# Performance work log

Measured on AMD Instinct MI355X. Metric: run time of the kernel, lower is better.

Reference implementation:

```python
import jax, jax.numpy as jnp
import numpy as np

N, L, H, V = 8192, 512, 64, 50000
NUM_PARENT = 1024


def setup_inputs() -> dict:
    key = jax.random.key(0)
    ks = jax.random.split(key, 12)
    def mat(k, shape):
        return 0.1 * jax.random.normal(k, shape, dtype=jnp.float32)
    return {
        "x_word": jax.random.normal(ks[0], (N, L), dtype=jnp.float32),
        "x_index": jax.random.randint(ks[1], (N, L), 0, V),
        "tree": jax.random.randint(ks[2], (N, 2), 0, N),
        "num_parent": NUM_PARENT,
        "embedding": mat(ks[3], (V, H)),
        "W_z": mat(ks[4], (H, H)),
        "U_z": mat(ks[5], (H, H)),
        "b_z": jnp.zeros((H,), dtype=jnp.float32),
        "W_r": mat(ks[6], (H, H)),
        "U_r": mat(ks[7], (H, H)),
        "b_r": jnp.zeros((H,), dtype=jnp.float32),
        "W_h": mat(ks[8], (H, H)),
        "U_h": mat(ks[9], (H, H)),
        "b_h": jnp.zeros((H,), dtype=jnp.float32),
    }


def _hard_sigmoid(x):
    # torch double-threshold trick == clip(0.2*x + 0.5, 0, 1)
    return jnp.clip(0.2 * x + 0.5, 0.0, 1.0)


def reference(x_word, x_index, tree, num_parent, embedding,
              W_z, U_z, b_z, W_r, U_r, b_r, W_h, U_h, b_h):
    n_nodes = x_word.shape[0]
    hdim = embedding.shape[1]

    def step(node_h, xs):
        word, idx, info = xs  # word: [L] f32, idx: [L] int, info: [2] int
        parent_h = node_h[info[0]]                 # [H]
        child_xe = embedding[idx].T @ word         # [H] weighted embedding sum
        z = _hard_sigmoid(W_z @ child_xe + U_z @ parent_h + b_z)
        r = _hard_sigmoid(W_r @ child_xe + U_r @ parent_h + b_r)
        c = jnp.tanh(W_h @ child_xe + U_h @ (parent_h * r) + b_h)
        h = z * parent_h + (1.0 - z) * c           # [H]
        return node_h.at[info[1]].set(h), h

    node_h0 = jnp.zeros((n_nodes, hdim), dtype=x_word.dtype)
    # original loops i in range(len(x_word) - 1)
    _, child_hs = jax.lax.scan(step, node_h0,
                               (x_word[:-1], x_index[:-1], tree[:-1]))
    # output = max over child_hs[num_parent-1:]
    return jnp.max(child_hs[num_parent - 1:], axis=0)
```

## Files before the change

### kernel.cpp

```cpp
#include <hip/hip_runtime.h>
#include <math.h>

#define NODES  8192
#define STEPS  8191
#define LW     512
#define H      64
#define VOCAB  50000
#define SWEEPK 4

typedef __attribute__((ext_vector_type(2))) float f32x2;

__global__ void ws_too_small_kernel(float* __restrict__ out) {
    if (threadIdx.x < H) out[threadIdx.x] = -12345.0f;
}

__global__ __launch_bounds__(256)
void cvt_emb(const float* __restrict__ emb, unsigned int* __restrict__ embq) {
    const int total = VOCAB * H / 4;
    for (int i = blockIdx.x * 256 + threadIdx.x; i < total; i += 256 * 256) {
        float4 v = reinterpret_cast<const float4*>(emb)[i];
        int w = 0;
        w = __builtin_amdgcn_cvt_pk_fp8_f32(v.x, v.y, w, false);
        w = __builtin_amdgcn_cvt_pk_fp8_f32(v.z, v.w, w, true);
        embq[i] = (unsigned int)w;
    }
}

__global__ __launch_bounds__(1024)
void build_schedule(const int* __restrict__ tree, int* __restrict__ writers_g,
                    int* __restrict__ pred_g, int* __restrict__ lstart_g,
                    int* __restrict__ order_g) {
    __shared__ int s_off[NODES + 8];
    __shared__ int wsum[16];
    int tid  = threadIdx.x;
    int lane = tid & 63;
    int wv   = tid >> 6;

    for (int i = tid; i < NODES + 8; i += 1024) s_off[i] = 0;
    __syncthreads();
    for (int j = tid; j < STEPS; j += 1024)
        atomicAdd(&s_off[tree[2 * j + 1]], 1);
    __syncthreads();

    {
        int base = tid * 8;
        int v[8], run = 0;
        #pragma unroll
        for (int e = 0; e < 8; ++e) { v[e] = run; run += s_off[base + e]; }
        int x = run;
        #pragma unroll
        for (int d = 1; d < 64; d <<= 1) {
            int y = __shfl_up(x, d, 64);
            if (lane >= d) x += y;
        }
        if (lane == 63) wsum[wv] = x;
        __syncthreads();
        if (wv == 0) {
            int s = (lane < 16) ? wsum[lane] : 0;
            #pragma unroll
            for (int d = 1; d < 16; d <<= 1) {
                int y = __shfl_up(s, d, 64);
                if (lane >= d) s += y;
            }
            if (lane < 16) wsum[lane] = s;
        }
        __syncthreads();
        int wbase = (wv > 0) ? wsum[wv - 1] : 0;
        int tbase = wbase + x - run;
        #pragma unroll
        for (int e = 0; e < 8; ++e) s_off[base + e] = tbase + v[e];
    }
    __syncthreads();

    for (int j = tid; j < STEPS; j += 1024) {
        int v = tree[2 * j + 1];
        int pos = atomicAdd(&s_off[v], 1);
        writers_g[pos] = j;
    }
    __syncthreads();

    int pr[8];
    #pragma unroll
    for (int e = 0; e < 8; ++e) {
        int i = tid + e * 1024;
        int best = -1;
        if (i < STEPS) {
            int v  = tree[2 * i];
            int t1 = s_off[v];
            int t0 = (v > 0) ? s_off[v - 1] : 0;
            for (int t = t0; t < t1; ++t) {
                int j = writers_g[t];
                if (j < i && j > best) best = j;
            }
            pred_g[i] = best;
        }
        pr[e] = best;
    }
    __syncthreads();

    short* jmp = (short*)s_off;
    short* dep = (short*)s_off + NODES;
    #pragma unroll
    for (int e = 0; e < 8; ++e) {
        int i = tid + e * 1024;
        jmp[i] = (short)pr[e];
        dep[i] = (pr[e] >= 0) ? 1 : 0;
    }
    __syncthreads();

    for (int r = 0; r < 13; ++r) {
        short nd[8], nj[8];
        #pragma unroll
        for (int e = 0; e < 8; ++e) {
            int i = tid + e * 1024;
            int j = jmp[i];
            if (j >= 0) { nd[e] = (short)(dep[i] + dep[j]); nj[e] = jmp[j]; }
            else        { nd[e] = dep[i];                   nj[e] = -1;     }
        }
        __syncthreads();
        #pragma unroll
        for (int e = 0; e < 8; ++e) {
            int i = tid + e * 1024;
            dep[i] = nd[e];
            jmp[i] = nj[e];
        }
        __syncthreads();
    }

    int d8[8];
    #pragma unroll
    for (int e = 0; e < 8; ++e) d8[e] = dep[tid + e * 1024];
    __syncthreads();

    int* lcnt = s_off;
    for (int i = tid; i < NODES; i += 1024) lcnt[i] = 0;
    __syncthreads();
    #pragma unroll
    for (int e = 0; e < 8; ++e) {
        int i = tid + e * 1024;
        if (i < STEPS) atomicAdd(&lcnt[d8[e]], 1);
    }
    __syncthreads();
    {
        int base = tid * 8;
        int v[8], run = 0;
        #pragma unroll
        for (int e = 0; e < 8; ++e) { v[e] = run; run += lcnt[base + e]; }
        int x = run;
        #pragma unroll
        for (int d = 1; d < 64; d <<= 1) {
            int y = __shfl_up(x, d, 64);
            if (lane >= d) x += y;
        }
        if (lane == 63) wsum[wv] = x;
        __syncthreads();
        if (wv == 0) {
            int s = (lane < 16) ? wsum[lane] : 0;
            #pragma unroll
            for (int d = 1; d < 16; d <<= 1) {
                int y = __shfl_up(s, d, 64);
                if (lane >= d) s += y;
            }
            if (lane < 16) wsum[lane] = s;
        }
        __syncthreads();
        int wbase = (wv > 0) ? wsum[wv - 1] : 0;
        int tbase = wbase + x - run;
        #pragma unroll
        for (int e = 0; e < 8; ++e) lstart_g[base + e] = tbase + v[e];
        if (tid == 1023) lstart_g[8192] = tbase + run;
    }
    __threadfence_block();
    __syncthreads();

    for (int i = tid; i < NODES; i += 1024) lcnt[i] = 0;
    __syncthreads();
    #pragma unroll
    for (int e = 0; e < 8; ++e) {
        int i = tid + e * 1024;
        if (i < STEPS) {
            int d = d8[e];
            int pos = atomicAdd(&lcnt[d], 1);
            order_g[lstart_g[d] + pos] = i;
        }
    }
}

__global__ __launch_bounds__(256)
void gather_project(const float* __restrict__ xw, const int* __restrict__ xi,
                    const unsigned int* __restrict__ embq,
                    const float* __restrict__ Wz, const float* __restrict__ Wr,
                    const float* __restrict__ Wh,
                    const float* __restrict__ bz, const float* __restrict__ br,
                    const float* __restrict__ bh,
                    const int* __restrict__ pred,
                    float* __restrict__ A, float* __restrict__ child_h) {
    int i    = blockIdx.x;
    int tid  = threadIdx.x;
    int wave = tid >> 6;
    int lane = tid & 63;
    int g16  = lane >> 2;
    int q4   = lane & 3;

    __shared__ float s_w[LW];
    __shared__ int   s_idx[LW];
    __shared__ float part[4][64];
    __shared__ float xe[64];

    {
        float2 w2 = reinterpret_cast<const float2*>(xw + (size_t)i * LW)[tid];
        int2   i2 = reinterpret_cast<const int2*>(xi + (size_t)i * LW)[tid];
        s_w[2 * tid]     = w2.x;
        s_w[2 * tid + 1] = w2.y;
        s_idx[2 * tid]     = i2.x;
        s_idx[2 * tid + 1] = i2.y;
    }
    __syncthreads();

    const uint4* E = reinterpret_cast<const uint4*>(embq);
    int base_l = wave * 128 + g16;

    float acc[16];
    #pragma unroll
    for (int c = 0; c < 16; ++c) acc[c] = 0.f;

    uint4 q[8];
    float wgt[8];
    #pragma unroll
    for (int u = 0; u < 8; ++u) {
        int l   = base_l + u * 16;
        int idx = s_idx[l];
        wgt[u]  = s_w[l];
        q[u]    = E[(size_t)idx * 4 + q4];
    }
    #pragma unroll
    for (int u = 0; u < 8; ++u) {
        float w = wgt[u];
        unsigned int uw[4] = {q[u].x, q[u].y, q[u].z, q[u].w};
        #pragma unroll
        for (int d = 0; d < 4; ++d) {
            f32x2 lo = __builtin_amdgcn_cvt_pk_f32_fp8((int)uw[d], false);
            f32x2 hi = __builtin_amdgcn_cvt_pk_f32_fp8((int)uw[d], true);
            acc[4 * d + 0] = fmaf(w, lo.x, acc[4 * d + 0]);
            acc[4 * d + 1] = fmaf(w, lo.y, acc[4 * d + 1]);
            acc[4 * d + 2] = fmaf(w, hi.x, acc[4 * d + 2]);
            acc[4 * d + 3] = fmaf(w, hi.y, acc[4 * d + 3]);
        }
    }
    #pragma unroll
    for (int c = 0; c < 16; ++c) {
        acc[c] += __shfl_xor(acc[c], 4,  64);
        acc[c] += __shfl_xor(acc[c], 8,  64);
        acc[c] += __shfl_xor(acc[c], 16, 64);
        acc[c] += __shfl_xor(acc[c], 32, 64);
    }
    if (lane < 4) {
        #pragma unroll
        for (int c = 0; c < 16; ++c) part[wave][lane * 16 + c] = acc[c];
    }
    __syncthreads();
    if (tid < 64) xe[tid] = part[0][tid] + part[1][tid] + part[2][tid] + part[3][tid];
    __syncthreads();

    float s = 0.f;
    if (tid < 192) {
        int o = tid & 63;
        const float* W = (tid < 64) ? Wz : (tid < 128 ? Wr : Wh);
        const float* b = (tid < 64) ? bz : (tid < 128 ? br : bh);
        s = b[o];
        #pragma unroll
        for (int j = 0; j < H; j += 4) {
            float4 w4 = *reinterpret_cast<const float4*>(W + (size_t)o * H + j);
            s = fmaf(w4.x, xe[j],     s);
            s = fmaf(w4.y, xe[j + 1], s);
            s = fmaf(w4.z, xe[j + 2], s);
            s = fmaf(w4.w, xe[j + 3], s);
        }
    }
    bool isroot = (pred[i] < 0);
    if (tid < 64)                part[0][tid]       = s;
    if (tid >= 128 && tid < 192) part[1][tid - 128] = s;
    __syncthreads();
    if (isroot) {
        if (tid < 64) {
            float z = fminf(fmaxf(0.2f * part[0][tid] + 0.5f, 0.f), 1.f);
            float c = tanhf(part[1][tid]);
            child_h[(size_t)i * H + tid] = (1.f - z) * c;
        }
    } else {
        if (tid < 192) A[(size_t)i * 192 + tid] = s;
    }
}

__device__ __forceinline__ float rlane(float v, int j) {
    return __int_as_float(__builtin_amdgcn_readlane(__float_as_int(v), j));
}

__device__ __forceinline__ void gru_core(
        int i, int lane, const float* __restrict__ A,
        const int* __restrict__ pred,
        const float* uz, const float* ur, const float* uh,
        float* __restrict__ child_h) {
    int p = pred[i];
    float ph = (p >= 0) ? child_h[(size_t)p * H + lane] : 0.f;
    const float* Ai = A + (size_t)i * 192;
    float az = Ai[lane];
    float ar = Ai[64 + lane];
    float ah = Ai[128 + lane];

    #pragma unroll
    for (int j = 0; j < H; ++j) {
        float s = rlane(ph, j);
        az = fmaf(uz[j], s, az);
        ar = fmaf(ur[j], s, ar);
    }
    float z = fminf(fmaxf(0.2f * az + 0.5f, 0.f), 1.f);
    float r = fminf(fmaxf(0.2f * ar + 0.5f, 0.f), 1.f);
    float phr = ph * r;
    #pragma unroll
    for (int j = 0; j < H; ++j) {
        float s = rlane(phr, j);
        ah = fmaf(uh[j], s, ah);
    }
    float c = tanhf(ah);
    child_h[(size_t)i * H + lane] = z * ph + (1.f - z) * c;
}

__global__ __launch_bounds__(256)
void sweep_lvl(int k, const int* __restrict__ lstart, const int* __restrict__ order,
               const float* __restrict__ A, const int* __restrict__ pred,
               const float* __restrict__ Uz, const float* __restrict__ Ur,
               const float* __restrict__ Uh, float* __restrict__ child_h) {
    int s0 = lstart[k], s1 = lstart[k + 1];
    int wave = (blockIdx.x * blockDim.x + threadIdx.x) >> 6;
    int lane = threadIdx.x & 63;
    if (s0 + wave >= s1) return;

    float uz[H], ur[H], uh[H];
    #pragma unroll
    for (int j = 0; j < H; j += 4) {
        float4 a4 = *reinterpret_cast<const float4*>(Uz + (size_t)lane * H + j);
        uz[j] = a4.x; uz[j+1] = a4.y; uz[j+2] = a4.z; uz[j+3] = a4.w;
        float4 b4 = *reinterpret_cast<const float4*>(Ur + (size_t)lane * H + j);
        ur[j] = b4.x; ur[j+1] = b4.y; ur[j+2] = b4.z; ur[j+3] = b4.w;
        float4 c4 = *reinterpret_cast<const float4*>(Uh + (size_t)lane * H + j);
        uh[j] = c4.x; uh[j+1] = c4.y; uh[j+2] = c4.z; uh[j+3] = c4.w;
    }
    for (int t = s0 + wave; t < s1; t += 512)
        gru_core(order[t], lane, A, pred, uz, ur, uh, child_h);
}

__global__ __launch_bounds__(512)
void tail_block(const int* __restrict__ lstart, const int* __restrict__ order,
                const float* __restrict__ A, const int* __restrict__ pred,
                const float* __restrict__ Uz, const float* __restrict__ Ur,
                const float* __restrict__ Uh, float* __restrict__ child_h) {
    int wave = threadIdx.x >> 6;
    int lane = threadIdx.x & 63;

    float uz[H], ur[H], uh[H];
    #pragma unroll
    for (int j = 0; j < H; j += 4) {
        float4 a4 = *reinterpret_cast<const float4*>(Uz + (size_t)lane * H + j);
        uz[j] = a4.x; uz[j+1] = a4.y; uz[j+2] = a4.z; uz[j+3] = a4.w;
        float4 b4 = *reinterpret_cast<const float4*>(Ur + (size_t)lane * H + j);
        ur[j] = b4.x; ur[j+1] = b4.y; ur[j+2] = b4.z; ur[j+3] = b4.w;
        float4 c4 = *reinterpret_cast<const float4*>(Uh + (size_t)lane * H + j);
        uh[j] = c4.x; uh[j+1] = c4.y; uh[j+2] = c4.z; uh[j+3] = c4.w;
    }

    for (int k = SWEEPK; k < NODES; ++k) {
        int s0 = lstart[k];
        if (s0 >= STEPS) break;
        int s1 = lstart[k + 1];
        for (int t = s0 + wave; t < s1; t += 8)
            gru_core(order[t], lane, A, pred, uz, ur, uh, child_h);
        __syncthreads();
    }
}

__global__ __launch_bounds__(256)
void reduce_partial(const float* __restrict__ child_h,
                    const int* __restrict__ np_ptr,
                    float* __restrict__ partial) {
    int b   = blockIdx.x;
    int tid = threadIdx.x;
    int h   = tid & 63;
    int grp = tid >> 6;
    int np    = *np_ptr;
    int start = np - 1;
    int total = STEPS - start;
    int per   = (total + gridDim.x - 1) / gridDim.x;
    int r0 = start + b * per;
    int r1 = r0 + per; if (r1 > STEPS) r1 = STEPS;
    float m = -INFINITY;
    for (int row = r0 + grp; row < r1; row += 4)
        m = fmaxf(m, child_h[(size_t)row * H + h]);
    __shared__ float sm[4][64];
    sm[grp][h] = m;
    __syncthreads();
    if (tid < 64)
        partial[b * 64 + tid] = fmaxf(fmaxf(sm[0][tid], sm[1][tid]),
                                      fmaxf(sm[2][tid], sm[3][tid]));
}

__global__ void reduce_final(const float* __restrict__ partial,
                             float* __restrict__ out, int nb) {
    int h = threadIdx.x;
    float m = -INFINITY;
    for (int b = 0; b < nb; ++b) m = fmaxf(m, partial[b * 64 + h]);
    out[h] = m;
}

extern "C" void kernel_launch(void* const* d_in, const int* in_sizes, int n_in,
                              void* d_out, int out_size, void* d_ws, size_t ws_size,
                              hipStream_t stream) {
    const float* xw   = (const float*)d_in[0];
    const int*   xi   = (const int*)  d_in[1];
    const int*   tree = (const int*)  d_in[2];
    const int*   np   = (const int*)  d_in[3];
    const float* emb  = (const float*)d_in[4];
    const float* Wz   = (const float*)d_in[5];
    const float* Uz   = (const float*)d_in[6];
    const float* bz   = (const float*)d_in[7];
    const float* Wr   = (const float*)d_in[8];
    const float* Ur   = (const float*)d_in[9];
    const float* br   = (const float*)d_in[10];
    const float* Wh   = (const float*)d_in[11];
    const float* Uh   = (const float*)d_in[12];
    const float* bh   = (const float*)d_in[13];

    size_t bA   = (size_t)STEPS * 192 * 4;
    size_t bCH  = (size_t)STEPS * H   * 4;
    size_t bEH  = (size_t)VOCAB * H   * 1;
    size_t bInt = (size_t)(8192 * 3 + 8256) * 4;
    size_t bPar = 56 * 64 * 4 + 256;
    size_t need = bA + bCH + bEH + bInt + bPar;
    if (ws_size < need) {
        ws_too_small_kernel<<<1, 64, 0, stream>>>((float*)d_out);
        return;
    }

    char* base = (char*)d_ws;
    float*          A       = (float*)base;                 base += bA;
    float*          child_h = (float*)base;                 base += bCH;
    unsigned int*   embq    = (unsigned int*)base;          base += bEH;
    int*            pred    = (int*)base;
    int*            writers = pred    + 8192;
    int*            order   = writers + 8192;
    int*            lstart  = order   + 8192;
    float*          partial = (float*)(lstart + 8256);

    cvt_emb        <<<256, 256, 0, stream>>>(emb, embq);

    build_schedule <<<1,  1024, 0, stream>>>(tree, writers, pred, lstart, order);

    gather_project <<<STEPS, 256, 0, stream>>>(xw, xi, embq, Wz, Wr, Wh,
                                               bz, br, bh, pred, A, child_h);

    for (int k = 1; k < SWEEPK; ++k)
        sweep_lvl  <<<128, 256, 0, stream>>>(k, lstart, order, A, pred,
                                             Uz, Ur, Uh, child_h);
    tail_block     <<<1, 512, 0, stream>>>(lstart, order, A, pred,
                                           Uz, Ur, Uh, child_h);

    reduce_partial <<<56,  256, 0, stream>>>(child_h, np, partial);
    reduce_final   <<<1,    64, 0, stream>>>(partial, (float*)d_out, 56);
}
```

Measured before the change: 288.1 us.

## Overlap schedule construction with gather by merging into one launch

The single-block dependency-schedule build moves into block 0 of the gather/projection kernel, so the serial schedule work runs alongside the 8191 gather blocks instead of before them. Because gather no longer knows pred, it always writes A, and a new root_steps kernel computes root hidden states afterwards. The sweep level count also rises from 4 to 6. The schedule block now runs with only 256 threads and larger per-thread register arrays, which may make that path longer, and it adds one extra launch plus the A reads for roots.

After: 319.9 us. +11.1%, slower.

```diff
diff --git a/kernel.cpp b/kernel.cpp
--- a/kernel.cpp
+++ b/kernel.cpp
@@ -6,7 +6,7 @@
 #define LW     512
 #define H      64
 #define VOCAB  50000
-#define SWEEPK 4
+#define SWEEPK 6
 
 typedef __attribute__((ext_vector_type(2))) float f32x2;
 
@@ -26,186 +26,168 @@
     }
 }
 
-__global__ __launch_bounds__(1024)
-void build_schedule(const int* __restrict__ tree, int* __restrict__ writers_g,
-                    int* __restrict__ pred_g, int* __restrict__ lstart_g,
-                    int* __restrict__ order_g) {
-    __shared__ int s_off[NODES + 8];
-    __shared__ int wsum[16];
-    int tid  = threadIdx.x;
-    int lane = tid & 63;
-    int wv   = tid >> 6;
-
-    for (int i = tid; i < NODES + 8; i += 1024) s_off[i] = 0;
-    __syncthreads();
-    for (int j = tid; j < STEPS; j += 1024)
-        atomicAdd(&s_off[tree[2 * j + 1]], 1);
-    __syncthreads();
-
-    {
-        int base = tid * 8;
-        int v[8], run = 0;
-        #pragma unroll
-        for (int e = 0; e < 8; ++e) { v[e] = run; run += s_off[base + e]; }
-        int x = run;
-        #pragma unroll
-        for (int d = 1; d < 64; d <<= 1) {
-            int y = __shfl_up(x, d, 64);
-            if (lane >= d) x += y;
-        }
-        if (lane == 63) wsum[wv] = x;
-        __syncthreads();
-        if (wv == 0) {
-            int s = (lane < 16) ? wsum[lane] : 0;
-            #pragma unroll
-            for (int d = 1; d < 16; d <<= 1) {
-                int y = __shfl_up(s, d, 64);
-                if (lane >= d) s += y;
-            }
-            if (lane < 16) wsum[lane] = s;
-        }
-        __syncthreads();
-        int wbase = (wv > 0) ? wsum[wv - 1] : 0;
-        int tbase = wbase + x - run;
-        #pragma unroll
-        for (int e = 0; e < 8; ++e) s_off[base + e] = tbase + v[e];
-    }
-    __syncthreads();
-
-    for (int j = tid; j < STEPS; j += 1024) {
-        int v = tree[2 * j + 1];
-        int pos = atomicAdd(&s_off[v], 1);
-        writers_g[pos] = j;
-    }
-    __syncthreads();
-
-    int pr[8];
-    #pragma unroll
-    for (int e = 0; e < 8; ++e) {
-        int i = tid + e * 1024;
-        int best = -1;
-        if (i < STEPS) {
-            int v  = tree[2 * i];
-            int t1 = s_off[v];
-            int t0 = (v > 0) ? s_off[v - 1] : 0;
-            for (int t = t0; t < t1; ++t) {
-                int j = writers_g[t];
-                if (j < i && j > best) best = j;
-            }
-            pred_g[i] = best;
-        }
-        pr[e] = best;
-    }
-    __syncthreads();
-
-    short* jmp = (short*)s_off;
-    short* dep = (short*)s_off + NODES;
-    #pragma unroll
-    for (int e = 0; e < 8; ++e) {
-        int i = tid + e * 1024;
-        jmp[i] = (short)pr[e];
-        dep[i] = (pr[e] >= 0) ? 1 : 0;
-    }
-    __syncthreads();
-
-    for (int r = 0; r < 13; ++r) {
-        short nd[8], nj[8];
-        #pragma unroll
-        for (int e = 0; e < 8; ++e) {
-            int i = tid + e * 1024;
-            int j = jmp[i];
-            if (j >= 0) { nd[e] = (short)(dep[i] + dep[j]); nj[e] = jmp[j]; }
-            else        { nd[e] = dep[i];                   nj[e] = -1;     }
-        }
-        __syncthreads();
-        #pragma unroll
-        for (int e = 0; e < 8; ++e) {
-            int i = tid + e * 1024;
-            dep[i] = nd[e];
-            jmp[i] = nj[e];
-        }
-        __syncthreads();
-    }
-
-    int d8[8];
-    #pragma unroll
-    for (int e = 0; e < 8; ++e) d8[e] = dep[tid + e * 1024];
-    __syncthreads();
-
-    int* lcnt = s_off;
-    for (int i = tid; i < NODES; i += 1024) lcnt[i] = 0;
-    __syncthreads();
-    #pragma unroll
-    for (int e = 0; e < 8; ++e) {
-        int i = tid + e * 1024;
-        if (i < STEPS) atomicAdd(&lcnt[d8[e]], 1);
-    }
-    __syncthreads();
-    {
-        int base = tid * 8;
-        int v[8], run = 0;
-        #pragma unroll
-        for (int e = 0; e < 8; ++e) { v[e] = run; run += lcnt[base + e]; }
-        int x = run;
-        #pragma unroll
-        for (int d = 1; d < 64; d <<= 1) {
-            int y = __shfl_up(x, d, 64);
-            if (lane >= d) x += y;
-        }
-        if (lane == 63) wsum[wv] = x;
-        __syncthreads();
-        if (wv == 0) {
-            int s = (lane < 16) ? wsum[lane] : 0;
-            #pragma unroll
-            for (int d = 1; d < 16; d <<= 1) {
-                int y = __shfl_up(s, d, 64);
-                if (lane >= d) s += y;
-            }
-            if (lane < 16) wsum[lane] = s;
-        }
-        __syncthreads();
-        int wbase = (wv > 0) ? wsum[wv - 1] : 0;
-        int tbase = wbase + x - run;
-        #pragma unroll
-        for (int e = 0; e < 8; ++e) lstart_g[base + e] = tbase + v[e];
-        if (tid == 1023) lstart_g[8192] = tbase + run;
-    }
-    __threadfence_block();
-    __syncthreads();
-
-    for (int i = tid; i < NODES; i += 1024) lcnt[i] = 0;
-    __syncthreads();
-    #pragma unroll
-    for (int e = 0; e < 8; ++e) {
-        int i = tid + e * 1024;
-        if (i < STEPS) {
-            int d = d8[e];
-            int pos = atomicAdd(&lcnt[d], 1);
-            order_g[lstart_g[d] + pos] = i;
-        }
-    }
-}
-
 __global__ __launch_bounds__(256)
-void gather_project(const float* __restrict__ xw, const int* __restrict__ xi,
-                    const unsigned int* __restrict__ embq,
-                    const float* __restrict__ Wz, const float* __restrict__ Wr,
-                    const float* __restrict__ Wh,
-                    const float* __restrict__ bz, const float* __restrict__ br,
-                    const float* __restrict__ bh,
-                    const int* __restrict__ pred,
-                    float* __restrict__ A, float* __restrict__ child_h) {
-    int i    = blockIdx.x;
-    int tid  = threadIdx.x;
+void gather_sched(const float* __restrict__ xw, const int* __restrict__ xi,
+                  const unsigned int* __restrict__ embq,
+                  const float* __restrict__ Wz, const float* __restrict__ Wr,
+                  const float* __restrict__ Wh,
+                  const float* __restrict__ bz, const float* __restrict__ br,
+                  const float* __restrict__ bh,
+                  const int* __restrict__ tree,
+                  float* __restrict__ A,
+                  int* __restrict__ writers_g, int* __restrict__ pred_g,
+                  int* __restrict__ lstart_g, int* __restrict__ order_g) {
+    __shared__ int smem[NODES + 8];
+    __shared__ int wsum[4];
+    int tid = threadIdx.x;
+
+    if (blockIdx.x == 0) {
+        int lane = tid & 63, wv = tid >> 6;
+
+        for (int i = tid; i < NODES + 8; i += 256) smem[i] = 0;
+        __syncthreads();
+        for (int j = tid; j < STEPS; j += 256)
+            atomicAdd(&smem[tree[2 * j + 1]], 1);
+        __syncthreads();
+
+        {
+            int base = tid * 32;
+            int v[32], run = 0;
+            #pragma unroll
+            for (int e = 0; e < 32; ++e) { v[e] = run; run += smem[base + e]; }
+            int x = run;
+            #pragma unroll
+            for (int d = 1; d < 64; d <<= 1) {
+                int y = __shfl_up(x, d, 64);
+                if (lane >= d) x += y;
+            }
+            if (lane == 63) wsum[wv] = x;
+            __syncthreads();
+            if (tid == 0) {
+                int a = 0;
+                for (int k = 0; k < 4; ++k) { a += wsum[k]; wsum[k] = a; }
+            }
+            __syncthreads();
+            int wbase = (wv > 0) ? wsum[wv - 1] : 0;
+            int tbase = wbase + x - run;
+            #pragma unroll
+            for (int e = 0; e < 32; ++e) smem[base + e] = tbase + v[e];
+        }
+        __syncthreads();
+
+        for (int j = tid; j < STEPS; j += 256) {
+            int v = tree[2 * j + 1];
+            int pos = atomicAdd(&smem[v], 1);
+            writers_g[pos] = j;
+        }
+        __syncthreads();
+
+        for (int e = 0; e < 32; ++e) {
+            int i = tid + e * 256;
+            if (i < STEPS) {
+                int v  = tree[2 * i];
+                int t1 = smem[v];
+                int t0 = (v > 0) ? smem[v - 1] : 0;
+                int best = -1;
+                for (int t = t0; t < t1; ++t) {
+                    int j = writers_g[t];
+                    if (j < i && j > best) best = j;
+                }
+                pred_g[i] = best;
+            }
+        }
+        __syncthreads();
+
+        short* jmp = (short*)smem;
+        short* dep = (short*)smem + NODES;
+        for (int e = 0; e < 32; ++e) {
+            int i = tid + e * 256;
+            int p = (i < STEPS) ? pred_g[i] : -1;
+            jmp[i] = (short)p;
+            dep[i] = (p >= 0) ? 1 : 0;
+        }
+        __syncthreads();
+        for (int r = 0; r < 13; ++r) {
+            short nd[32], nj[32];
+            #pragma unroll
+            for (int e = 0; e < 32; ++e) {
+                int i = tid + e * 256;
+                int j = jmp[i];
+                if (j >= 0) { nd[e] = (short)(dep[i] + dep[j]); nj[e] = jmp[j]; }
+                else        { nd[e] = dep[i];                   nj[e] = -1;     }
+            }
+            __syncthreads();
+            #pragma unroll
+            for (int e = 0; e < 32; ++e) {
+                int i = tid + e * 256;
+                dep[i] = nd[e];
+                jmp[i] = nj[e];
+            }
+            __syncthreads();
+        }
+        short d32[32];
+        #pragma unroll
+        for (int e = 0; e < 32; ++e) d32[e] = dep[tid + e * 256];
+        __syncthreads();
+
+        for (int i = tid; i < NODES; i += 256) smem[i] = 0;
+        __syncthreads();
+        #pragma unroll
+        for (int e = 0; e < 32; ++e) {
+            int i = tid + e * 256;
+            if (i < STEPS) atomicAdd(&smem[d32[e]], 1);
+        }
+        __syncthreads();
+        {
+            int base = tid * 32;
+            int v[32], run = 0;
+            #pragma unroll
+            for (int e = 0; e < 32; ++e) { v[e] = run; run += smem[base + e]; }
+            int x = run;
+            #pragma unroll
+            for (int d = 1; d < 64; d <<= 1) {
+                int y = __shfl_up(x, d, 64);
+                if (lane >= d) x += y;
+            }
+            if (lane == 63) wsum[wv] = x;
+            __syncthreads();
+            if (tid == 0) {
+                int a = 0;
+                for (int k = 0; k < 4; ++k) { a += wsum[k]; wsum[k] = a; }
+            }
+            __syncthreads();
+            int wbase = (wv > 0) ? wsum[wv - 1] : 0;
+            int tbase = wbase + x - run;
+            #pragma unroll
+            for (int e = 0; e < 32; ++e) lstart_g[base + e] = tbase + v[e];
+            if (tid == 255) lstart_g[8192] = tbase + run;
+        }
+        __threadfence_block();
+        __syncthreads();
+        for (int i = tid; i < NODES; i += 256) smem[i] = 0;
+        __syncthreads();
+        #pragma unroll
+        for (int e = 0; e < 32; ++e) {
+            int i = tid + e * 256;
+            if (i < STEPS) {
+                int d = d32[e];
+                int pos = atomicAdd(&smem[d], 1);
+                order_g[lstart_g[d] + pos] = i;
+            }
+        }
+        return;
+    }
+
+    int i    = blockIdx.x - 1;
     int wave = tid >> 6;
     int lane = tid & 63;
     int g16  = lane >> 2;
     int q4   = lane & 3;
 
-    __shared__ float s_w[LW];
-    __shared__ int   s_idx[LW];
-    __shared__ float part[4][64];
-    __shared__ float xe[64];
+    float* s_w   = (float*)smem;
+    int*   s_idx = smem + 512;
+    float* partf = (float*)(smem + 1024);
+    float* xe    = (float*)(smem + 1024 + 256);
 
     {
         float2 w2 = reinterpret_cast<const float2*>(xw + (size_t)i * LW)[tid];
@@ -256,18 +238,18 @@
     }
     if (lane < 4) {
         #pragma unroll
-        for (int c = 0; c < 16; ++c) part[wave][lane * 16 + c] = acc[c];
+        for (int c = 0; c < 16; ++c) partf[wave * 64 + lane * 16 + c] = acc[c];
     }
     __syncthreads();
-    if (tid < 64) xe[tid] = part[0][tid] + part[1][tid] + part[2][tid] + part[3][tid];
+    if (tid < 64)
+        xe[tid] = partf[tid] + partf[64 + tid] + partf[128 + tid] + partf[192 + tid];
     __syncthreads();
 
-    float s = 0.f;
     if (tid < 192) {
         int o = tid & 63;
         const float* W = (tid < 64) ? Wz : (tid < 128 ? Wr : Wh);
         const float* b = (tid < 64) ? bz : (tid < 128 ? br : bh);
-        s = b[o];
+        float s = b[o];
         #pragma unroll
         for (int j = 0; j < H; j += 4) {
             float4 w4 = *reinterpret_cast<const float4*>(W + (size_t)o * H + j);
@@ -276,20 +258,22 @@
             s = fmaf(w4.z, xe[j + 2], s);
             s = fmaf(w4.w, xe[j + 3], s);
         }
-    }
-    bool isroot = (pred[i] < 0);
-    if (tid < 64)                part[0][tid]       = s;
-    if (tid >= 128 && tid < 192) part[1][tid - 128] = s;
-    __syncthreads();
-    if (isroot) {
-        if (tid < 64) {
-            float z = fminf(fmaxf(0.2f * part[0][tid] + 0.5f, 0.f), 1.f);
-            float c = tanhf(part[1][tid]);
-            child_h[(size_t)i * H + tid] = (1.f - z) * c;
-        }
-    } else {
-        if (tid < 192) A[(size_t)i * 192 + tid] = s;
-    }
+        A[(size_t)i * 192 + tid] = s;
+    }
+}
+
+__global__ __launch_bounds__(256)
+void root_steps(const float* __restrict__ A, const int* __restrict__ pred,
+                float* __restrict__ child_h) {
+    int s = blockIdx.x * 4 + (threadIdx.x >> 6);
+    int h = threadIdx.x & 63;
+    if (s >= STEPS) return;
+    if (pred[s] >= 0) return;
+    float az = A[(size_t)s * 192 + h];
+    float ah = A[(size_t)s * 192 + 128 + h];
+    float z = fminf(fmaxf(0.2f * az + 0.5f, 0.f), 1.f);
+    float c = tanhf(ah);
+    child_h[(size_t)s * H + h] = (1.f - z) * c;
 }
 
 __device__ __forceinline__ float rlane(float v, int j) {
@@ -453,10 +437,11 @@
 
     cvt_emb        <<<256, 256, 0, stream>>>(emb, embq);
 
-    build_schedule <<<1,  1024, 0, stream>>>(tree, writers, pred, lstart, order);
-
-    gather_project <<<STEPS, 256, 0, stream>>>(xw, xi, embq, Wz, Wr, Wh,
-                                               bz, br, bh, pred, A, child_h);
+    gather_sched   <<<8192, 256, 0, stream>>>(xw, xi, embq, Wz, Wr, Wh,
+                                              bz, br, bh, tree, A,
+                                              writers, pred, lstart, order);
+
+    root_steps     <<<2048, 256, 0, stream>>>(A, pred, child_h);
 
     for (int k = 1; k < SWEEPK; ++k)
         sweep_lvl  <<<128, 256, 0, stream>>>(k, lstart, order, A, pred,
```
